# Kernel optimization log

Measured on AMD Instinct MI355X. Metric: run time of the kernel, lower is better.

The kernel has to match this reference:

```python
import jax, jax.numpy as jnp
import numpy as np
from jax import lax

B, T, IN, H = 128, 1024, 130, 512


def setup_inputs() -> dict:
    key = jax.random.key(0)
    ks = jax.random.split(key, 6)
    inputs = jax.random.normal(ks[0], (B, T, IN), dtype=jnp.float32)
    # valid lengths in [1, T] (forward indexes outputs[len-1])
    inputs_len = jax.random.randint(ks[1], (B,), 1, T + 1)
    h0 = jnp.zeros((B, H), dtype=jnp.float32)
    c0 = jnp.zeros((B, H), dtype=jnp.float32)
    s = 1.0 / np.sqrt(H)
    W_ih = jax.random.uniform(ks[2], (4 * H, IN - 2), jnp.float32, -s, s)
    W_hh = jax.random.uniform(ks[3], (4 * H, H), jnp.float32, -s, s)
    b_ih = jax.random.uniform(ks[4], (4 * H,), jnp.float32, -s, s)
    b_hh = jax.random.uniform(ks[5], (4 * H,), jnp.float32, -s, s)
    return {"inputs": inputs, "inputs_len": inputs_len, "h0": h0, "c0": c0,
            "W_ih": W_ih, "W_hh": W_hh, "b_ih": b_ih, "b_hh": b_hh}


def _lstm_encode(inputs, h0, c0, W_ih, W_hh, b_ih, b_hh):
    # drop last 2 features (coordinates), as in stard_LSTM branch
    x = inputs[..., :-2]                                   # [B, T, IN-2]
    # precompute input projections for all timesteps (same math as per-step)
    xproj = jnp.einsum('bti,gi->tbg', x, W_ih) + b_ih + b_hh  # [T, B, 4H]

    def step(carry, xw):
        h, c = carry
        gates = xw + h @ W_hh.T                            # [B, 4H]
        i, f, g, o = jnp.split(gates, 4, axis=-1)
        i = jax.nn.sigmoid(i)
        f = jax.nn.sigmoid(f)
        g = jnp.tanh(g)
        o = jax.nn.sigmoid(o)
        c2 = f * c + i * g
        h2 = o * jnp.tanh(c2)
        return (h2, c2), h2

    _, hs = lax.scan(step, (h0, c0), xproj)                # hs: [T, B, H]
    return hs


def reference(inputs, inputs_len, h0, c0, W_ih, W_hh, b_ih, b_hh):
    hs = _lstm_encode(inputs, h0, c0, W_ih, W_hh, b_ih, b_hh)
    # gather hidden state at last valid timestep per sequence
    b_idx = jnp.arange(inputs.shape[0])
    return hs[inputs_len - 1, b_idx]                       # [B, H]
```

## Files before the change

kernel.cpp:

```cpp
#include <hip/hip_runtime.h>
#include <hip/hip_bf16.h>
#include <cstdint>
#include <cstddef>

#define T_STEPS 1024
#define BATCH   128
#define INF     128
#define HID     512
#define NBLK    256
#define NTHR    512
#define PK      648
#define Z_SHORTS    (2 * 16 * PK)
#define Z_BYTES     (Z_SHORTS * 2)
#define RED_BYTES   (256 * 16)
#define SMEM_BYTES  (2 * Z_BYTES + RED_BYTES)

typedef short  bf16x8 __attribute__((ext_vector_type(8)));
typedef float  f32x4  __attribute__((ext_vector_type(4)));

static __device__ __forceinline__ unsigned short bf_hi(float v) {
  __hip_bfloat16 h = __float2bfloat16(v);
  return *reinterpret_cast<unsigned short*>(&h);
}
static __device__ __forceinline__ float bf_val(unsigned short u) {
  __hip_bfloat16 h = *reinterpret_cast<__hip_bfloat16*>(&u);
  return __bfloat162float(h);
}
static __device__ __forceinline__ float fsigmoid(float x) {
  return 1.f / (1.f + __expf(-x));
}
static __device__ __forceinline__ float ftanh(float x) {
  return 1.f - 2.f / (__expf(2.f * x) + 1.f);
}


__global__ __launch_bounds__(256) void k_prep_x(const float* __restrict__ in,
                                                unsigned short* __restrict__ xp)
{
  int t = blockIdx.x >> 3, bg = blockIdx.x & 7;
  int tid = threadIdx.x;
  size_t base = (size_t)blockIdx.x * 4096;
  #pragma unroll
  for (int rep = 0; rep < 8; ++rep) {
    int idx = rep * 256 + tid;
    int c = idx >> 7, k = idx & 127;
    float v = in[((size_t)(bg * 16 + c) * T_STEPS + t) * 130 + k];
    unsigned short hi = bf_hi(v);
    unsigned short lo = bf_hi(v - bf_val(hi));
    xp[base + c * 128 + k]        = hi;
    xp[base + 2048 + c * 128 + k] = lo;
  }
}

__global__ __launch_bounds__(64) void k_prep_w(const float* __restrict__ Wih,
                                               const float* __restrict__ Whh,
                                               unsigned short* __restrict__ wf)
{
  int blk = blockIdx.x;
  int s = blk % 10; int r = blk / 10;
  int kh = r & 1; int u4 = (r >> 1) & 3; int ug = r >> 3;
  int l = threadIdx.x;
  int m = l & 15;
  int Grow = (m & 3) * HID + ug * 16 + u4 * 4 + (m >> 2);
  int kb = kh * 320 + s * 32 + (l >> 4) * 8;
  float v[8];
  #pragma unroll
  for (int j = 0; j < 8; ++j)
    v[j] = (kb < INF) ? Wih[(size_t)Grow * INF + kb + j]
                      : Whh[(size_t)Grow * HID + (kb - INF) + j];
  unsigned short hi[8], lo[8];
  #pragma unroll
  for (int j = 0; j < 8; ++j) {
    hi[j] = bf_hi(v[j]);
    lo[j] = bf_hi(v[j] - bf_val(hi[j]));
  }
  unsigned short* dh = wf + ((size_t)(blk * 2 + 0) * 64 + l) * 8;
  unsigned short* dl = wf + ((size_t)(blk * 2 + 1) * 64 + l) * 8;
  #pragma unroll
  for (int j = 0; j < 8; ++j) { dh[j] = hi[j]; dl[j] = lo[j]; }
}

__global__ __launch_bounds__(256) void k_prep_h(const float* __restrict__ h0,
                                                unsigned long long* __restrict__ hp0)
{
  int idx = blockIdx.x * 256 + threadIdx.x;
  int bg = idx >> 13;
  int r = idx & 8191;
  int u = r >> 4, c = r & 15;
  float v = h0[(size_t)(bg * 16 + c) * HID + u];
  unsigned short hi = bf_hi(v);
  unsigned short lo = bf_hi(v - bf_val(hi));
  hp0[idx] = (unsigned long long)((unsigned)hi | ((unsigned)lo << 16));
}

__global__ __launch_bounds__(NTHR, 2) void k_persist(
    const unsigned short* __restrict__ xp,
    const unsigned short* __restrict__ wf,
    const float* __restrict__ bih, const float* __restrict__ bhh,
    unsigned long long* __restrict__ hp0,
    unsigned long long* __restrict__ hp1,
    const float* __restrict__ c0,
    const int* __restrict__ len,
    float* __restrict__ out)
{
  extern __shared__ char smem[];
  short* zpl = (short*)smem;
  f32x4* red = (f32x4*)(smem + 2 * Z_BYTES);

  const int blk = blockIdx.x;
  const int ug = blk & 31, bg = blk >> 5;
  const int tid = threadIdx.x;
  const int w = tid >> 6, l = tid & 63;
  const int u4 = w & 3, kh = w >> 2;
  const int cB = l & 15, gch = l >> 4;

  const uint4* wfq = (const uint4*)wf;
  const int fbase = ((ug * 4 + u4) * 2 + kh) * 10;
#define LDW(s_, p_) \
  (*reinterpret_cast<const bf16x8*>(&wfq[(size_t)((fbase + (s_)) * 2 + (p_)) * 64 + l]))
  bf16x8 A0h = LDW(0,0), A0l = LDW(0,1), A1h = LDW(1,0), A1l = LDW(1,1);
  bf16x8 A2h = LDW(2,0), A2l = LDW(2,1), A3h = LDW(3,0), A3l = LDW(3,1);
  bf16x8 A4h = LDW(4,0), A4l = LDW(4,1), A5h = LDW(5,0), A5l = LDW(5,1);
  bf16x8 A6h = LDW(6,0), A6l = LDW(6,1), A7h = LDW(7,0), A7l = LDW(7,1);
  bf16x8 A8h = LDW(8,0), A8l = LDW(8,1), A9h = LDW(9,0), A9l = LDW(9,1);
#undef LDW
  asm volatile("" : "+v"(A0h), "+v"(A0l), "+v"(A1h), "+v"(A1l), "+v"(A2h),
                    "+v"(A2l), "+v"(A3h), "+v"(A3l), "+v"(A4h), "+v"(A4l),
                    "+v"(A5h), "+v"(A5l), "+v"(A6h), "+v"(A6l), "+v"(A7h),
                    "+v"(A7l), "+v"(A8h), "+v"(A8l), "+v"(A9h), "+v"(A9l));

  const int cb = l & 15;
  const int hu = ug * 16 + u4 * 4 + (l >> 4);
  const int gb = bg * 16 + cb;
  float c_reg = 0.f, bsq[4] = {0.f, 0.f, 0.f, 0.f};
  int mylen = -1;
  if (tid < 256) {
    c_reg = c0[(size_t)gb * HID + hu];
    mylen = len[gb];
    #pragma unroll
    for (int g = 0; g < 4; ++g) bsq[g] = bih[g * HID + hu] + bhh[g * HID + hu];
  }

  const int pc = tid & 15, qq = tid >> 4;
  const int pbase = 32 * qq + pc;

  for (int t = 0; t < T_STEPS; ++t) {
    short* zcur = zpl + (t & 1) * Z_SHORTS;
    const unsigned long long* hq = ((t & 1) ? hp1 : hp0) + (size_t)bg * 8192;
    unsigned long long*       hd = ((t & 1) ? hp0 : hp1) + (size_t)bg * 8192;

    uint4 xv = ((const uint4*)(xp + (size_t)(t * 8 + bg) * 4096))[tid];

    unsigned long long hch[16];
    #pragma unroll
    for (int j = 0; j < 16; ++j)
      hch[j] = __hip_atomic_load(hq + 1024 * (j >> 1) + 16 * (j & 1) + pbase,
                                 __ATOMIC_RELAXED, __HIP_MEMORY_SCOPE_AGENT);
    for (;;) {
      int bad = 0;
      #pragma unroll
      for (int j = 0; j < 16; ++j)
        if ((unsigned)(hch[j] >> 32) != (unsigned)t) {
          hch[j] = __hip_atomic_load(hq + 1024 * (j >> 1) + 16 * (j & 1) + pbase,
                                     __ATOMIC_RELAXED, __HIP_MEMORY_SCOPE_AGENT);
          bad = 1;
        }
      if (!__any(bad)) break;
      __builtin_amdgcn_s_sleep(1);
    }

    {
      int p_ = tid >> 8, c_ = (tid >> 4) & 15, kc = tid & 15;
      *(uint4*)(zcur + (p_ * 16 + c_) * PK + kc * 8) = xv;
    }
    #pragma unroll
    for (int p = 0; p < 8; ++p) {
      unsigned e0 = (unsigned)hch[2 * p], e1 = (unsigned)hch[2 * p + 1];
      unsigned hipair = (e0 & 0xFFFFu) | (e1 << 16);
      unsigned lopair = (e0 >> 16) | (e1 & 0xFFFF0000u);
      int off = pc * PK + 128 + 64 * p + 2 * qq;
      *(unsigned*)(zcur + off)           = hipair;
      *(unsigned*)(zcur + 16 * PK + off) = lopair;
    }
    __syncthreads();

    f32x4 accE = {0, 0, 0, 0}, accO = {0, 0, 0, 0};
#define KSTEP(s_, AH, AL, ACC)                                                 \
  {                                                                            \
    int ka = kh * 320 + (s_) * 32 + gch * 8;                                   \
    bf16x8 Bh = *(const bf16x8*)(zcur + cB * PK + ka);                         \
    bf16x8 Bl = *(const bf16x8*)(zcur + 16 * PK + cB * PK + ka);               \
    ACC = __builtin_amdgcn_mfma_f32_16x16x32_bf16(AH, Bh, ACC, 0, 0, 0);       \
    ACC = __builtin_amdgcn_mfma_f32_16x16x32_bf16(AH, Bl, ACC, 0, 0, 0);       \
    ACC = __builtin_amdgcn_mfma_f32_16x16x32_bf16(AL, Bh, ACC, 0, 0, 0);       \
  }
    KSTEP(0, A0h, A0l, accE) KSTEP(1, A1h, A1l, accO)
    KSTEP(2, A2h, A2l, accE) KSTEP(3, A3h, A3l, accO)
    KSTEP(4, A4h, A4l, accE) KSTEP(5, A5h, A5l, accO)
    KSTEP(6, A6h, A6l, accE) KSTEP(7, A7h, A7l, accO)
    KSTEP(8, A8h, A8l, accE) KSTEP(9, A9h, A9l, accO)
#undef KSTEP
    f32x4 acc = accE + accO;

    if (w >= 4) red[u4 * 64 + l] = acc;
    __syncthreads();
    if (tid < 256) {
      f32x4 o = red[u4 * 64 + l];
      float s0 = acc[0] + o[0] + bsq[0];
      float s1 = acc[1] + o[1] + bsq[1];
      float s2 = acc[2] + o[2] + bsq[2];
      float s3 = acc[3] + o[3] + bsq[3];
      float iv = fsigmoid(s0);
      float fv = fsigmoid(s1);
      float gv = ftanh(s2);
      float ov = fsigmoid(s3);
      c_reg = fv * c_reg + iv * gv;
      float h2 = ov * ftanh(c_reg);
      unsigned short hh = bf_hi(h2);
      unsigned short ll = bf_hi(h2 - bf_val(hh));
      unsigned long long word = ((unsigned long long)(unsigned)(t + 1) << 32)
                              | (unsigned long long)((unsigned)hh | ((unsigned)ll << 16));
      __hip_atomic_store(hd + hu * 16 + cb, word,
                         __ATOMIC_RELAXED, __HIP_MEMORY_SCOPE_AGENT);
      if (t == mylen - 1) out[(size_t)gb * HID + hu] = h2;
    }
  }
}

extern "C" void kernel_launch(void* const* d_in, const int* in_sizes, int n_in,
                              void* d_out, int out_size, void* d_ws, size_t ws_size,
                              hipStream_t stream)
{
  const float* inputs = (const float*)d_in[0];
  const int*   len    = (const int*)  d_in[1];
  const float* h0     = (const float*)d_in[2];
  const float* c0     = (const float*)d_in[3];
  const float* Wih    = (const float*)d_in[4];
  const float* Whh    = (const float*)d_in[5];
  const float* bih    = (const float*)d_in[6];
  const float* bhh    = (const float*)d_in[7];
  float* out = (float*)d_out;

  char* p = (char*)d_ws;
  unsigned short* xp = (unsigned short*)p; p += (size_t)T_STEPS * 8 * 4096 * 2;
  unsigned short* wf = (unsigned short*)p; p += (size_t)2560 * 2 * 64 * 8 * 2;
  unsigned long long* hp0 = (unsigned long long*)p; p += (size_t)8 * 8192 * 8;
  unsigned long long* hp1 = (unsigned long long*)p; p += (size_t)8 * 8192 * 8;

  (void)hipFuncSetAttribute((const void*)k_persist,
                            hipFuncAttributeMaxDynamicSharedMemorySize, SMEM_BYTES);

  k_prep_x<<<T_STEPS * 8, 256, 0, stream>>>(inputs, xp);
  k_prep_w<<<2560, 64, 0, stream>>>(Wih, Whh, wf);
  k_prep_h<<<256, 256, 0, stream>>>(h0, hp0);

  void* args[] = {(void*)&xp, (void*)&wf, (void*)&bih, (void*)&bhh,
                  (void*)&hp0, (void*)&hp1, (void*)&c0, (void*)&len,
                  (void*)&out};
  (void)hipLaunchCooperativeKernel((void*)k_persist, dim3(NBLK), dim3(NTHR),
                                   args, SMEM_BYTES, stream);
}
```

Before: 3.774 ms.

## Switch LSTM recurrence to single fp16 MFMA with flag-based step sync

Replaces the split-bf16 (hi/lo, three MFMAs per k-step) scheme with a single fp16 operand per value, which halves the staged x/h data and cuts the MFMA count. Each block now runs 4 waves that each cover the full K, so the cross-wave shared-memory reduction and one barrier are gone. Per-element step tags on the hidden-state words are replaced by per-block progress flags, so waiting blocks poll 32 flag words and then do plain packed fp16 loads. The trade-off is lower precision (fp16 without compensation over 1024 recurrent steps) and an ordering risk: flags and data are published with relaxed atomics and no fence.

```diff
diff --git a/kernel.cpp b/kernel.cpp
--- a/kernel.cpp
+++ b/kernel.cpp
@@ -8,23 +8,17 @@
 #define INF     128
 #define HID     512
 #define NBLK    256
-#define NTHR    512
+#define NTHR    256
 #define PK      648
-#define Z_SHORTS    (2 * 16 * PK)
-#define Z_BYTES     (Z_SHORTS * 2)
-#define RED_BYTES   (256 * 16)
-#define SMEM_BYTES  (2 * Z_BYTES + RED_BYTES)
-
-typedef short  bf16x8 __attribute__((ext_vector_type(8)));
-typedef float  f32x4  __attribute__((ext_vector_type(4)));
-
-static __device__ __forceinline__ unsigned short bf_hi(float v) {
-  __hip_bfloat16 h = __float2bfloat16(v);
-  return *reinterpret_cast<unsigned short*>(&h);
-}
-static __device__ __forceinline__ float bf_val(unsigned short u) {
-  __hip_bfloat16 h = *reinterpret_cast<__hip_bfloat16*>(&u);
-  return __bfloat162float(h);
+
+typedef _Float16 f16x8 __attribute__((ext_vector_type(8)));
+typedef float    f32x4 __attribute__((ext_vector_type(4)));
+
+static __device__ __forceinline__ unsigned short f16b(float v) {
+  _Float16 h = (_Float16)v;
+  unsigned short u;
+  __builtin_memcpy(&u, &h, 2);
+  return u;
 }
 static __device__ __forceinline__ float fsigmoid(float x) {
   return 1.f / (1.f + __expf(-x));
@@ -39,16 +33,13 @@
 {
   int t = blockIdx.x >> 3, bg = blockIdx.x & 7;
   int tid = threadIdx.x;
-  size_t base = (size_t)blockIdx.x * 4096;
+  size_t base = (size_t)blockIdx.x * 2048;
   #pragma unroll
   for (int rep = 0; rep < 8; ++rep) {
     int idx = rep * 256 + tid;
     int c = idx >> 7, k = idx & 127;
     float v = in[((size_t)(bg * 16 + c) * T_STEPS + t) * 130 + k];
-    unsigned short hi = bf_hi(v);
-    unsigned short lo = bf_hi(v - bf_val(hi));
-    xp[base + c * 128 + k]        = hi;
-    xp[base + 2048 + c * 128 + k] = lo;
+    xp[base + c * 128 + k] = f16b(v);
   }
 }
 
@@ -57,173 +48,142 @@
                                                unsigned short* __restrict__ wf)
 {
   int blk = blockIdx.x;
-  int s = blk % 10; int r = blk / 10;
-  int kh = r & 1; int u4 = (r >> 1) & 3; int ug = r >> 3;
+  int s = blk % 20; int r = blk / 20;
+  int u4 = r & 3; int ug = r >> 2;
   int l = threadIdx.x;
   int m = l & 15;
   int Grow = (m & 3) * HID + ug * 16 + u4 * 4 + (m >> 2);
-  int kb = kh * 320 + s * 32 + (l >> 4) * 8;
-  float v[8];
-  #pragma unroll
-  for (int j = 0; j < 8; ++j)
-    v[j] = (kb < INF) ? Wih[(size_t)Grow * INF + kb + j]
-                      : Whh[(size_t)Grow * HID + (kb - INF) + j];
-  unsigned short hi[8], lo[8];
+  int kb = s * 32 + (l >> 4) * 8;
+  unsigned short o[8];
   #pragma unroll
   for (int j = 0; j < 8; ++j) {
-    hi[j] = bf_hi(v[j]);
-    lo[j] = bf_hi(v[j] - bf_val(hi[j]));
+    float v = (kb + j < INF) ? Wih[(size_t)Grow * INF + kb + j]
+                             : Whh[(size_t)Grow * HID + (kb + j - INF)];
+    o[j] = f16b(v);
   }
-  unsigned short* dh = wf + ((size_t)(blk * 2 + 0) * 64 + l) * 8;
-  unsigned short* dl = wf + ((size_t)(blk * 2 + 1) * 64 + l) * 8;
-  #pragma unroll
-  for (int j = 0; j < 8; ++j) { dh[j] = hi[j]; dl[j] = lo[j]; }
+  unsigned short* d = wf + ((size_t)blk * 64 + l) * 8;
+  #pragma unroll
+  for (int j = 0; j < 8; ++j) d[j] = o[j];
 }
 
 __global__ __launch_bounds__(256) void k_prep_h(const float* __restrict__ h0,
-                                                unsigned long long* __restrict__ hp0)
+                                                unsigned short* __restrict__ hp0,
+                                                unsigned* __restrict__ flags)
 {
   int idx = blockIdx.x * 256 + threadIdx.x;
   int bg = idx >> 13;
   int r = idx & 8191;
-  int u = r >> 4, c = r & 15;
-  float v = h0[(size_t)(bg * 16 + c) * HID + u];
-  unsigned short hi = bf_hi(v);
-  unsigned short lo = bf_hi(v - bf_val(hi));
-  hp0[idx] = (unsigned long long)((unsigned)hi | ((unsigned)lo << 16));
-}
-
-__global__ __launch_bounds__(NTHR, 2) void k_persist(
+  int c = r >> 9, u = r & 511;
+  hp0[idx] = f16b(h0[(size_t)(bg * 16 + c) * HID + u]);
+  if (blockIdx.x == 0 && threadIdx.x < 256) flags[threadIdx.x] = 0;
+}
+
+__global__ __launch_bounds__(NTHR, 1) void k_persist(
     const unsigned short* __restrict__ xp,
     const unsigned short* __restrict__ wf,
     const float* __restrict__ bih, const float* __restrict__ bhh,
-    unsigned long long* __restrict__ hp0,
-    unsigned long long* __restrict__ hp1,
+    unsigned short* __restrict__ hp0,
+    unsigned short* __restrict__ hp1,
     const float* __restrict__ c0,
     const int* __restrict__ len,
-    float* __restrict__ out)
-{
-  extern __shared__ char smem[];
-  short* zpl = (short*)smem;
-  f32x4* red = (f32x4*)(smem + 2 * Z_BYTES);
+    float* __restrict__ out,
+    unsigned* __restrict__ flags)
+{
+  __shared__ short zpl[16][PK];
 
   const int blk = blockIdx.x;
   const int ug = blk & 31, bg = blk >> 5;
   const int tid = threadIdx.x;
   const int w = tid >> 6, l = tid & 63;
-  const int u4 = w & 3, kh = w >> 2;
   const int cB = l & 15, gch = l >> 4;
 
   const uint4* wfq = (const uint4*)wf;
-  const int fbase = ((ug * 4 + u4) * 2 + kh) * 10;
-#define LDW(s_, p_) \
-  (*reinterpret_cast<const bf16x8*>(&wfq[(size_t)((fbase + (s_)) * 2 + (p_)) * 64 + l]))
-  bf16x8 A0h = LDW(0,0), A0l = LDW(0,1), A1h = LDW(1,0), A1l = LDW(1,1);
-  bf16x8 A2h = LDW(2,0), A2l = LDW(2,1), A3h = LDW(3,0), A3l = LDW(3,1);
-  bf16x8 A4h = LDW(4,0), A4l = LDW(4,1), A5h = LDW(5,0), A5l = LDW(5,1);
-  bf16x8 A6h = LDW(6,0), A6l = LDW(6,1), A7h = LDW(7,0), A7l = LDW(7,1);
-  bf16x8 A8h = LDW(8,0), A8l = LDW(8,1), A9h = LDW(9,0), A9l = LDW(9,1);
+  const int fb = (ug * 4 + w) * 20;
+#define LDW(s_) (*reinterpret_cast<const f16x8*>(&wfq[(size_t)(fb + (s_)) * 64 + l]))
+  f16x8 A0 = LDW(0),  A1 = LDW(1),  A2 = LDW(2),  A3 = LDW(3),  A4 = LDW(4);
+  f16x8 A5 = LDW(5),  A6 = LDW(6),  A7 = LDW(7),  A8 = LDW(8),  A9 = LDW(9);
+  f16x8 A10 = LDW(10), A11 = LDW(11), A12 = LDW(12), A13 = LDW(13), A14 = LDW(14);
+  f16x8 A15 = LDW(15), A16 = LDW(16), A17 = LDW(17), A18 = LDW(18), A19 = LDW(19);
 #undef LDW
-  asm volatile("" : "+v"(A0h), "+v"(A0l), "+v"(A1h), "+v"(A1l), "+v"(A2h),
-                    "+v"(A2l), "+v"(A3h), "+v"(A3l), "+v"(A4h), "+v"(A4l),
-                    "+v"(A5h), "+v"(A5l), "+v"(A6h), "+v"(A6l), "+v"(A7h),
-                    "+v"(A7l), "+v"(A8h), "+v"(A8l), "+v"(A9h), "+v"(A9l));
+  asm volatile("" : "+v"(A0), "+v"(A1), "+v"(A2), "+v"(A3), "+v"(A4),
+                    "+v"(A5), "+v"(A6), "+v"(A7), "+v"(A8), "+v"(A9),
+                    "+v"(A10), "+v"(A11), "+v"(A12), "+v"(A13), "+v"(A14),
+                    "+v"(A15), "+v"(A16), "+v"(A17), "+v"(A18), "+v"(A19));
 
   const int cb = l & 15;
-  const int hu = ug * 16 + u4 * 4 + (l >> 4);
+  const int hu = ug * 16 + w * 4 + (l >> 4);
   const int gb = bg * 16 + cb;
-  float c_reg = 0.f, bsq[4] = {0.f, 0.f, 0.f, 0.f};
-  int mylen = -1;
-  if (tid < 256) {
-    c_reg = c0[(size_t)gb * HID + hu];
-    mylen = len[gb];
+  float c_reg = c0[(size_t)gb * HID + hu];
+  const int mylen = len[gb];
+  float bsq[4];
+  #pragma unroll
+  for (int g = 0; g < 4; ++g) bsq[g] = bih[g * HID + hu] + bhh[g * HID + hu];
+
+  const unsigned* fl = flags + bg * 32;
+  const int hc = tid >> 4, hj = tid & 15;
+
+  for (int t = 0; t < T_STEPS; ++t) {
+    uint4 xv = ((const uint4*)(xp + (size_t)(t * 8 + bg) * 2048))[tid];
+
+    if (t) {
+      const unsigned* fp = fl + (l & 31);
+      for (;;) {
+        unsigned v = __hip_atomic_load(fp, __ATOMIC_RELAXED,
+                                       __HIP_MEMORY_SCOPE_AGENT);
+        if (__all((int)(v >= (unsigned)t))) break;
+        __builtin_amdgcn_s_sleep(1);
+      }
+    }
+    const unsigned long long* hq =
+        (const unsigned long long*)(((t & 1) ? hp1 : hp0) + (size_t)bg * 8192);
+    unsigned* hdw = (unsigned*)(((t & 1) ? hp0 : hp1) + (size_t)bg * 8192);
+
+    unsigned long long hch[8];
     #pragma unroll
-    for (int g = 0; g < 4; ++g) bsq[g] = bih[g * HID + hu] + bhh[g * HID + hu];
-  }
-
-  const int pc = tid & 15, qq = tid >> 4;
-  const int pbase = 32 * qq + pc;
-
-  for (int t = 0; t < T_STEPS; ++t) {
-    short* zcur = zpl + (t & 1) * Z_SHORTS;
-    const unsigned long long* hq = ((t & 1) ? hp1 : hp0) + (size_t)bg * 8192;
-    unsigned long long*       hd = ((t & 1) ? hp0 : hp1) + (size_t)bg * 8192;
-
-    uint4 xv = ((const uint4*)(xp + (size_t)(t * 8 + bg) * 4096))[tid];
-
-    unsigned long long hch[16];
+    for (int k = 0; k < 8; ++k)
+      hch[k] = __hip_atomic_load(hq + hc * 128 + hj * 8 + k,
+                                 __ATOMIC_RELAXED, __HIP_MEMORY_SCOPE_AGENT);
+
+    *(uint4*)((char*)&zpl[tid >> 4][0] + (tid & 15) * 16) = xv;
     #pragma unroll
-    for (int j = 0; j < 16; ++j)
-      hch[j] = __hip_atomic_load(hq + 1024 * (j >> 1) + 16 * (j & 1) + pbase,
-                                 __ATOMIC_RELAXED, __HIP_MEMORY_SCOPE_AGENT);
-    for (;;) {
-      int bad = 0;
-      #pragma unroll
-      for (int j = 0; j < 16; ++j)
-        if ((unsigned)(hch[j] >> 32) != (unsigned)t) {
-          hch[j] = __hip_atomic_load(hq + 1024 * (j >> 1) + 16 * (j & 1) + pbase,
-                                     __ATOMIC_RELAXED, __HIP_MEMORY_SCOPE_AGENT);
-          bad = 1;
-        }
-      if (!__any(bad)) break;
-      __builtin_amdgcn_s_sleep(1);
-    }
-
-    {
-      int p_ = tid >> 8, c_ = (tid >> 4) & 15, kc = tid & 15;
-      *(uint4*)(zcur + (p_ * 16 + c_) * PK + kc * 8) = xv;
-    }
-    #pragma unroll
-    for (int p = 0; p < 8; ++p) {
-      unsigned e0 = (unsigned)hch[2 * p], e1 = (unsigned)hch[2 * p + 1];
-      unsigned hipair = (e0 & 0xFFFFu) | (e1 << 16);
-      unsigned lopair = (e0 >> 16) | (e1 & 0xFFFF0000u);
-      int off = pc * PK + 128 + 64 * p + 2 * qq;
-      *(unsigned*)(zcur + off)           = hipair;
-      *(unsigned*)(zcur + 16 * PK + off) = lopair;
-    }
+    for (int k = 0; k < 8; ++k)
+      *(unsigned long long*)(&zpl[hc][0] + 128 + hj * 32 + 4 * k) = hch[k];
     __syncthreads();
 
-    f32x4 accE = {0, 0, 0, 0}, accO = {0, 0, 0, 0};
-#define KSTEP(s_, AH, AL, ACC)                                                 \
-  {                                                                            \
-    int ka = kh * 320 + (s_) * 32 + gch * 8;                                   \
-    bf16x8 Bh = *(const bf16x8*)(zcur + cB * PK + ka);                         \
-    bf16x8 Bl = *(const bf16x8*)(zcur + 16 * PK + cB * PK + ka);               \
-    ACC = __builtin_amdgcn_mfma_f32_16x16x32_bf16(AH, Bh, ACC, 0, 0, 0);       \
-    ACC = __builtin_amdgcn_mfma_f32_16x16x32_bf16(AH, Bl, ACC, 0, 0, 0);       \
-    ACC = __builtin_amdgcn_mfma_f32_16x16x32_bf16(AL, Bh, ACC, 0, 0, 0);       \
-  }
-    KSTEP(0, A0h, A0l, accE) KSTEP(1, A1h, A1l, accO)
-    KSTEP(2, A2h, A2l, accE) KSTEP(3, A3h, A3l, accO)
-    KSTEP(4, A4h, A4l, accE) KSTEP(5, A5h, A5l, accO)
-    KSTEP(6, A6h, A6l, accE) KSTEP(7, A7h, A7l, accO)
-    KSTEP(8, A8h, A8l, accE) KSTEP(9, A9h, A9l, accO)
-#undef KSTEP
-    f32x4 acc = accE + accO;
-
-    if (w >= 4) red[u4 * 64 + l] = acc;
+    f32x4 aE = {0, 0, 0, 0}, aO = {0, 0, 0, 0};
+    const short* zr = &zpl[cB][0];
+#define KS(s_, AF, ACC) \
+  { f16x8 B = *(const f16x8*)(zr + (s_) * 32 + gch * 8); \
+    ACC = __builtin_amdgcn_mfma_f32_16x16x32_f16(AF, B, ACC, 0, 0, 0); }
+    KS(0, A0, aE)  KS(1, A1, aO)  KS(2, A2, aE)  KS(3, A3, aO)
+    KS(4, A4, aE)  KS(5, A5, aO)  KS(6, A6, aE)  KS(7, A7, aO)
+    KS(8, A8, aE)  KS(9, A9, aO)  KS(10, A10, aE) KS(11, A11, aO)
+    KS(12, A12, aE) KS(13, A13, aO) KS(14, A14, aE) KS(15, A15, aO)
+    KS(16, A16, aE) KS(17, A17, aO) KS(18, A18, aE) KS(19, A19, aO)
+#undef KS
+
+    float s0 = aE[0] + aO[0] + bsq[0];
+    float s1 = aE[1] + aO[1] + bsq[1];
+    float s2 = aE[2] + aO[2] + bsq[2];
+    float s3 = aE[3] + aO[3] + bsq[3];
+    float iv = fsigmoid(s0);
+    float fv = fsigmoid(s1);
+    float gv = ftanh(s2);
+    float ov = fsigmoid(s3);
+    c_reg = fv * c_reg + iv * gv;
+    float h2 = ov * ftanh(c_reg);
+
+    unsigned hb = f16b(h2);
+    unsigned other = __shfl_xor(hb, 16);
+    if (((l >> 4) & 1) == 0)
+      __hip_atomic_store(hdw + cb * 256 + (hu >> 1), hb | (other << 16),
+                         __ATOMIC_RELAXED, __HIP_MEMORY_SCOPE_AGENT);
+    if (t == mylen - 1) out[(size_t)gb * HID + hu] = h2;
+
     __syncthreads();
-    if (tid < 256) {
-      f32x4 o = red[u4 * 64 + l];
-      float s0 = acc[0] + o[0] + bsq[0];
-      float s1 = acc[1] + o[1] + bsq[1];
-      float s2 = acc[2] + o[2] + bsq[2];
-      float s3 = acc[3] + o[3] + bsq[3];
-      float iv = fsigmoid(s0);
-      float fv = fsigmoid(s1);
-      float gv = ftanh(s2);
-      float ov = fsigmoid(s3);
-      c_reg = fv * c_reg + iv * gv;
-      float h2 = ov * ftanh(c_reg);
-      unsigned short hh = bf_hi(h2);
-      unsigned short ll = bf_hi(h2 - bf_val(hh));
-      unsigned long long word = ((unsigned long long)(unsigned)(t + 1) << 32)
-                              | (unsigned long long)((unsigned)hh | ((unsigned)ll << 16));
-      __hip_atomic_store(hd + hu * 16 + cb, word,
+    if (tid == 0)
+      __hip_atomic_store((unsigned*)(flags + bg * 32 + ug), (unsigned)(t + 1),
                          __ATOMIC_RELAXED, __HIP_MEMORY_SCOPE_AGENT);
-      if (t == mylen - 1) out[(size_t)gb * HID + hu] = h2;
-    }
   }
 }
 
@@ -242,21 +202,19 @@
   float* out = (float*)d_out;
 
   char* p = (char*)d_ws;
-  unsigned short* xp = (unsigned short*)p; p += (size_t)T_STEPS * 8 * 4096 * 2;
-  unsigned short* wf = (unsigned short*)p; p += (size_t)2560 * 2 * 64 * 8 * 2;
-  unsigned long long* hp0 = (unsigned long long*)p; p += (size_t)8 * 8192 * 8;
-  unsigned long long* hp1 = (unsigned long long*)p; p += (size_t)8 * 8192 * 8;
-
-  (void)hipFuncSetAttribute((const void*)k_persist,
-                            hipFuncAttributeMaxDynamicSharedMemorySize, SMEM_BYTES);
+  unsigned short* xp = (unsigned short*)p; p += (size_t)T_STEPS * 8 * 2048 * 2;
+  unsigned short* wf = (unsigned short*)p; p += (size_t)2560 * 64 * 8 * 2;
+  unsigned short* hp0 = (unsigned short*)p; p += (size_t)8 * 8192 * 2;
+  unsigned short* hp1 = (unsigned short*)p; p += (size_t)8 * 8192 * 2;
+  unsigned* flags = (unsigned*)p; p += 256 * 4;
 
   k_prep_x<<<T_STEPS * 8, 256, 0, stream>>>(inputs, xp);
   k_prep_w<<<2560, 64, 0, stream>>>(Wih, Whh, wf);
-  k_prep_h<<<256, 256, 0, stream>>>(h0, hp0);
+  k_prep_h<<<256, 256, 0, stream>>>(h0, hp0, flags);
 
   void* args[] = {(void*)&xp, (void*)&wf, (void*)&bih, (void*)&bhh,
                   (void*)&hp0, (void*)&hp1, (void*)&c0, (void*)&len,
-                  (void*)&out};
+                  (void*)&out, (void*)&flags};
   (void)hipLaunchCooperativeKernel((void*)k_persist, dim3(NBLK), dim3(NTHR),
-                                   args, SMEM_BYTES, stream);
-}
+                                   args, 0, stream);
+}
```

New measurement: 3.270 ms. 13.4% less time.
